# Kernel tuning notes

Hardware: AMD Instinct MI355X
Metric: run time of the kernel (lower is better)

The kernel has to match this reference:

```python
import jax, jax.numpy as jnp
import numpy as np

N, D, H = 8192, 1536, 1536


def setup_inputs() -> dict:
    key = jax.random.key(0)
    ks = jax.random.split(key, 7)
    def lin(kk, fan_in, fan_out):
        lim = 1.0 / np.sqrt(fan_in)
        return jax.random.uniform(kk, (fan_in, fan_out), jnp.float32, -lim, lim)
    return {
        "mentions": jax.random.normal(ks[0], (N, D), jnp.float32),
        "W0": lin(ks[1], D, H),
        "b0": jnp.zeros((H,), jnp.float32),
        "W1": lin(ks[2], H, H),
        "b1": jnp.zeros((H,), jnp.float32),
        "Wout": lin(ks[3], H, 1),
        "bout": jnp.zeros((1,), jnp.float32),
        "k": 50,
    }


def reference(mentions, W0, b0, W1, b1, Wout, bout, k):
    # MLP (dropout is identity at eval time); LeakyReLU slope 0.01 (torch default)
    h = jax.nn.leaky_relu(mentions @ W0 + b0, negative_slope=0.01)
    h = jax.nn.leaky_relu(h @ W1 + b1, negative_slope=0.01)
    s = (h @ Wout + bout).squeeze(-1)  # [N] per-mention scores
    n = s.shape[0]
    idx = jnp.arange(n)
    # pair_mask[i,j] = log(i - j > 0): 0 where j < i (valid antecedent), -inf otherwise
    pair_mask = jnp.where(idx[:, None] > idx[None, :], 0.0, -jnp.inf).astype(s.dtype)
    # scores_ij[i,j] = s[j] + s[i] + mask
    scores_ij = s[None, :] + s[:, None] + pair_mask
    top_scores, indices = jax.lax.top_k(scores_ij, min(int(k), n))
    return top_scores, indices
```

## Files before the change

### kernel.cpp

```cpp
#include <hip/hip_runtime.h>
#include <math.h>
#include <float.h>

#define BM 128
#define BN 128
#define BK 16
#define TM 8
#define TN 8
#define LDA_S (BM + 4)
#define LDB_S (BN + 16)

__device__ __forceinline__ int bpad(int c) { return c + ((c >> 5) << 2); }

__global__ __launch_bounds__(256) void sgemm_bias_act(
    const float* __restrict__ A, const float* __restrict__ W,
    const float* __restrict__ bias, float* __restrict__ C,
    int M, int K, int N)
{
    __shared__ float As[BK * LDA_S];
    __shared__ float Bs[BK * LDB_S];

    const int tid = threadIdx.x;
    const int bm = blockIdx.x;
    const int bn = blockIdx.y;

    const int tn = tid & 15;
    const int tm = tid >> 4;
    const int row0 = tm * TM;
    const int col0 = tn * TN;
    const int cs0 = bpad(col0);

    const int lr  = tid >> 2;
    const int lc4 = (tid & 3) << 2;
    const int br  = tid >> 5;
    const int bc4 = (tid & 31) << 2;
    const int bcs = bpad(bc4);

    const float* Ag = A + (size_t)(bm * BM) * K;
    const float* Wg = W + (size_t)bn * BN;

    float acc[TM][TN];
#pragma unroll
    for (int i = 0; i < TM; ++i)
#pragma unroll
        for (int j = 0; j < TN; ++j) acc[i][j] = 0.f;

    float4 a0 = *(const float4*)(Ag + (size_t)lr * K + lc4);
    float4 a1 = *(const float4*)(Ag + (size_t)(lr + 64) * K + lc4);
    float4 b0 = *(const float4*)(Wg + (size_t)br * N + bc4);
    float4 b1 = *(const float4*)(Wg + (size_t)(br + 8) * N + bc4);

    for (int k0 = 0; k0 < K; k0 += BK) {
        __syncthreads();
        As[(lc4 + 0) * LDA_S + lr] = a0.x;
        As[(lc4 + 1) * LDA_S + lr] = a0.y;
        As[(lc4 + 2) * LDA_S + lr] = a0.z;
        As[(lc4 + 3) * LDA_S + lr] = a0.w;
        As[(lc4 + 0) * LDA_S + lr + 64] = a1.x;
        As[(lc4 + 1) * LDA_S + lr + 64] = a1.y;
        As[(lc4 + 2) * LDA_S + lr + 64] = a1.z;
        As[(lc4 + 3) * LDA_S + lr + 64] = a1.w;
        *(float4*)&Bs[br * LDB_S + bcs] = b0;
        *(float4*)&Bs[(br + 8) * LDB_S + bcs] = b1;
        __syncthreads();

        if (k0 + BK < K) {
            const int kn = k0 + BK;
            a0 = *(const float4*)(Ag + (size_t)lr * K + kn + lc4);
            a1 = *(const float4*)(Ag + (size_t)(lr + 64) * K + kn + lc4);
            b0 = *(const float4*)(Wg + (size_t)(kn + br) * N + bc4);
            b1 = *(const float4*)(Wg + (size_t)(kn + br + 8) * N + bc4);
        }

#pragma unroll
        for (int kk = 0; kk < BK; ++kk) {
            float4 av0 = *(const float4*)&As[kk * LDA_S + row0];
            float4 av1 = *(const float4*)&As[kk * LDA_S + row0 + 4];
            float4 bv0 = *(const float4*)&Bs[kk * LDB_S + cs0];
            float4 bv1 = *(const float4*)&Bs[kk * LDB_S + cs0 + 4];
            float a[TM] = {av0.x, av0.y, av0.z, av0.w, av1.x, av1.y, av1.z, av1.w};
            float b[TN] = {bv0.x, bv0.y, bv0.z, bv0.w, bv1.x, bv1.y, bv1.z, bv1.w};
#pragma unroll
            for (int i = 0; i < TM; ++i)
#pragma unroll
                for (int j = 0; j < TN; ++j)
                    acc[i][j] = fmaf(a[i], b[j], acc[i][j]);
        }
    }

    float bv[TN];
#pragma unroll
    for (int j = 0; j < TN; ++j) bv[j] = bias[bn * BN + col0 + j];
#pragma unroll
    for (int i = 0; i < TM; ++i) {
        float o[TN];
#pragma unroll
        for (int j = 0; j < TN; ++j) {
            float x = acc[i][j] + bv[j];
            o[j] = x > 0.f ? x : 0.01f * x;
        }
        float* Cp = C + (size_t)(bm * BM + row0 + i) * N + (size_t)bn * BN + col0;
        *(float4*)Cp       = make_float4(o[0], o[1], o[2], o[3]);
        *(float4*)(Cp + 4) = make_float4(o[4], o[5], o[6], o[7]);
    }
}

__global__ __launch_bounds__(256) void gemv_wout(
    const float* __restrict__ H, const float* __restrict__ Wout,
    const float* __restrict__ bout, float* __restrict__ s, int K)
{
    const int row  = blockIdx.x * 4 + (threadIdx.x >> 6);
    const int lane = threadIdx.x & 63;
    const float4* h = (const float4*)(H + (size_t)row * K);
    const float4* w = (const float4*)Wout;
    float acc = 0.f;
    const int nv = K >> 2;
#pragma unroll
    for (int t = lane; t < nv; t += 64) {
        float4 hv = h[t];
        float4 wv = w[t];
        acc += hv.x * wv.x + hv.y * wv.y + hv.z * wv.z + hv.w * wv.w;
    }
#pragma unroll
    for (int off = 32; off; off >>= 1) acc += __shfl_xor(acc, off);
    if (lane == 0) s[row] = acc + bout[0];
}

#define EMPTY_SENTINEL (-1.0e38f)
#define HEAP_SENTINEL  (-1e30f)

__global__ void chunk_sort(const float* __restrict__ s,
                           float* __restrict__ cval, int* __restrict__ cidx)
{
    const int lane = threadIdx.x;
    const int base = blockIdx.x * 64;
    float v  = s[base + lane];
    int   id = base + lane;
#pragma unroll
    for (int ksz = 2; ksz <= 64; ksz <<= 1) {
#pragma unroll
        for (int j = 32; j >= 1; j >>= 1) {
            if (j >= ksz) continue;
            float ov = __shfl_xor(v, j);
            int   oi = __shfl_xor(id, j);
            const bool lower    = ((lane & j) == 0);
            const bool dirDesc  = ((lane & ksz) == 0);
            const bool wantBig  = (lower == dirDesc);
            const bool mineBig  = (v > ov) || (v == ov && id < oi);
            const bool keepMine = (mineBig == wantBig);
            v  = keepMine ? v  : ov;
            id = keepMine ? id : oi;
        }
    }
    cval[base + lane] = v;
    cidx[base + lane] = id;
}

__global__ void prefix_merge(const float* __restrict__ cval,
                             const int* __restrict__ cidx,
                             float* __restrict__ qval, int* __restrict__ qidx,
                             int nchunks)
{
    const int lane = threadIdx.x;
    float v  = HEAP_SENTINEL;
    int   id = 0x3FFFFFFF;
    for (int c = 0; c < nchunks; ++c) {
        qval[c * 64 + lane] = v;
        qidx[c * 64 + lane] = id;
        float bv = cval[c * 64 + (63 - lane)];
        int   bi = cidx[c * 64 + (63 - lane)];
        const bool mineBig0 = (v > bv) || (v == bv && id < bi);
        v  = mineBig0 ? v  : bv;
        id = mineBig0 ? id : bi;
#pragma unroll
        for (int j = 32; j >= 1; j >>= 1) {
            float ov = __shfl_xor(v, j);
            int   oi = __shfl_xor(id, j);
            const bool lower    = ((lane & j) == 0);
            const bool mineBig  = (v > ov) || (v == ov && id < oi);
            const bool keepMine = (mineBig == lower);
            v  = keepMine ? v  : ov;
            id = keepMine ? id : oi;
        }
    }
}

__global__ void topk_replay(const float* __restrict__ s,
                            const float* __restrict__ qval,
                            const int* __restrict__ qidx,
                            float* __restrict__ out_scores,
                            float* __restrict__ out_idx, int k)
{
    const int lane = threadIdx.x;
    const int c = blockIdx.x;
    float val = qval[c * 64 + lane];
    int   idx = qidx[c * 64 + lane];
    const float sv = s[c * 64 + lane];

    for (int t = 0; t < 64; ++t) {
        const int i = c * 64 + t;
        const float si = __shfl(sv, t);
        if (lane < k) {
            const bool empty = (lane >= i);
            out_scores[(size_t)i * k + lane] = empty ? EMPTY_SENTINEL : (si + val);
            out_idx[(size_t)i * k + lane]    = (float)(empty ? lane : idx);
        }
        unsigned long long ge = __ballot(val >= si);
        int p = __popcll(ge);
        float upv = __shfl_up(val, 1);
        int   upi = __shfl_up(idx, 1);
        if (lane > p)       { val = upv; idx = upi; }
        else if (lane == p) { val = si;  idx = i;   }
    }
}

extern "C" void kernel_launch(void* const* d_in, const int* in_sizes, int n_in,
                              void* d_out, int out_size, void* d_ws, size_t ws_size,
                              hipStream_t stream)
{
    const float* mentions = (const float*)d_in[0];
    const float* W0   = (const float*)d_in[1];
    const float* b0   = (const float*)d_in[2];
    const float* W1   = (const float*)d_in[3];
    const float* b1   = (const float*)d_in[4];
    const float* Wout = (const float*)d_in[5];
    const float* bout = (const float*)d_in[6];

    const int D = 1536, H = 1536;
    const int M = in_sizes[0] / D;
    const int k = out_size / (2 * M);
    const int NCH = M / 64;

    float* h0   = (float*)d_ws;
    float* h1   = h0 + (size_t)M * H;
    float* sc   = h1 + (size_t)M * H;
    float* cval = sc + M;
    int*   cidx = (int*)(cval + M);
    float* qval = (float*)(cidx + M);
    int*   qidx = (int*)(qval + M);

    dim3 g1(M / BM, H / BN);
    sgemm_bias_act<<<g1, 256, 0, stream>>>(mentions, W0, b0, h0, M, D, H);
    sgemm_bias_act<<<g1, 256, 0, stream>>>(h0, W1, b1, h1, M, H, H);
    gemv_wout<<<M / 4, 256, 0, stream>>>(h1, Wout, bout, sc, H);

    chunk_sort<<<NCH, 64, 0, stream>>>(sc, cval, cidx);
    prefix_merge<<<1, 64, 0, stream>>>(cval, cidx, qval, qidx, NCH);

    float* out_scores = (float*)d_out;
    float* out_idx    = (float*)d_out + (size_t)M * k;
    topk_replay<<<NCH, 64, 0, stream>>>(sc, qval, qidx, out_scores, out_idx, k);
}
```

Baseline: 1.077 ms.

## Double-buffer shared memory tiles in SGEMM to cut per-iteration barriers

Shared-memory A/B tiles in the fp32 GEMM become double buffered. Each step stores the already-loaded next tile into the other buffer and issues global loads two tiles ahead, so only one barrier per k-step is needed instead of two. This reduces synchronisation overhead and overlaps global latency with the FMA loop, at the cost of twice the LDS use, which may reduce occupancy, and more live registers.

```diff
diff --git a/kernel.cpp b/kernel.cpp
--- a/kernel.cpp
+++ b/kernel.cpp
@@ -17,8 +17,8 @@
     const float* __restrict__ bias, float* __restrict__ C,
     int M, int K, int N)
 {
-    __shared__ float As[BK * LDA_S];
-    __shared__ float Bs[BK * LDB_S];
+    __shared__ float As[2][BK * LDA_S];
+    __shared__ float Bs[2][BK * LDB_S];
 
     const int tid = threadIdx.x;
     const int bm = blockIdx.x;
@@ -45,47 +45,63 @@
 #pragma unroll
         for (int j = 0; j < TN; ++j) acc[i][j] = 0.f;
 
-    float4 a0 = *(const float4*)(Ag + (size_t)lr * K + lc4);
-    float4 a1 = *(const float4*)(Ag + (size_t)(lr + 64) * K + lc4);
-    float4 b0 = *(const float4*)(Wg + (size_t)br * N + bc4);
-    float4 b1 = *(const float4*)(Wg + (size_t)(br + 8) * N + bc4);
-
+    float4 a0, a1, b0, b1;
+#define LOAD_TILE(k0_)                                                        \
+    do {                                                                      \
+        a0 = *(const float4*)(Ag + (size_t)lr * K + (k0_) + lc4);             \
+        a1 = *(const float4*)(Ag + (size_t)(lr + 64) * K + (k0_) + lc4);      \
+        b0 = *(const float4*)(Wg + (size_t)((k0_) + br) * N + bc4);           \
+        b1 = *(const float4*)(Wg + (size_t)((k0_) + br + 8) * N + bc4);       \
+    } while (0)
+
+#define STORE_TILE(buf_)                                                      \
+    do {                                                                      \
+        As[buf_][(lc4 + 0) * LDA_S + lr] = a0.x;                              \
+        As[buf_][(lc4 + 1) * LDA_S + lr] = a0.y;                              \
+        As[buf_][(lc4 + 2) * LDA_S + lr] = a0.z;                              \
+        As[buf_][(lc4 + 3) * LDA_S + lr] = a0.w;                              \
+        As[buf_][(lc4 + 0) * LDA_S + lr + 64] = a1.x;                         \
+        As[buf_][(lc4 + 1) * LDA_S + lr + 64] = a1.y;                         \
+        As[buf_][(lc4 + 2) * LDA_S + lr + 64] = a1.z;                         \
+        As[buf_][(lc4 + 3) * LDA_S + lr + 64] = a1.w;                         \
+        *(float4*)&Bs[buf_][br * LDB_S + bcs] = b0;                           \
+        *(float4*)&Bs[buf_][(br + 8) * LDB_S + bcs] = b1;                     \
+    } while (0)
+
+    LOAD_TILE(0);
+    STORE_TILE(0);
+    if (BK < K) LOAD_TILE(BK);
+    __syncthreads();
+
+    int cur = 0;
     for (int k0 = 0; k0 < K; k0 += BK) {
+        if (k0 + BK < K) STORE_TILE(cur ^ 1);
+        if (k0 + 2 * BK < K) LOAD_TILE(k0 + 2 * BK);
+        const float* Ac = As[cur];
+        const float* Bc = Bs[cur];
+#pragma unroll
+        for (int kk = 0; kk < BK; ++kk) {
+            const float4 av0 = *(const float4*)&Ac[kk * LDA_S + row0];
+            const float4 av1 = *(const float4*)&Ac[kk * LDA_S + row0 + 4];
+            const float4 bv0 = *(const float4*)&Bc[kk * LDB_S + cs0];
+            const float4 bv1 = *(const float4*)&Bc[kk * LDB_S + cs0 + 4];
+#define FMA_ROW(i, ax)                                                        \
+            acc[i][0] = fmaf(ax, bv0.x, acc[i][0]);                           \
+            acc[i][1] = fmaf(ax, bv0.y, acc[i][1]);                           \
+            acc[i][2] = fmaf(ax, bv0.z, acc[i][2]);                           \
+            acc[i][3] = fmaf(ax, bv0.w, acc[i][3]);                           \
+            acc[i][4] = fmaf(ax, bv1.x, acc[i][4]);                           \
+            acc[i][5] = fmaf(ax, bv1.y, acc[i][5]);                           \
+            acc[i][6] = fmaf(ax, bv1.z, acc[i][6]);                           \
+            acc[i][7] = fmaf(ax, bv1.w, acc[i][7])
+            FMA_ROW(0, av0.x); FMA_ROW(1, av0.y);
+            FMA_ROW(2, av0.z); FMA_ROW(3, av0.w);
+            FMA_ROW(4, av1.x); FMA_ROW(5, av1.y);
+            FMA_ROW(6, av1.z); FMA_ROW(7, av1.w);
+#undef FMA_ROW
+        }
         __syncthreads();
-        As[(lc4 + 0) * LDA_S + lr] = a0.x;
-        As[(lc4 + 1) * LDA_S + lr] = a0.y;
-        As[(lc4 + 2) * LDA_S + lr] = a0.z;
-        As[(lc4 + 3) * LDA_S + lr] = a0.w;
-        As[(lc4 + 0) * LDA_S + lr + 64] = a1.x;
-        As[(lc4 + 1) * LDA_S + lr + 64] = a1.y;
-        As[(lc4 + 2) * LDA_S + lr + 64] = a1.z;
-        As[(lc4 + 3) * LDA_S + lr + 64] = a1.w;
-        *(float4*)&Bs[br * LDB_S + bcs] = b0;
-        *(float4*)&Bs[(br + 8) * LDB_S + bcs] = b1;
-        __syncthreads();
-
-        if (k0 + BK < K) {
-            const int kn = k0 + BK;
-            a0 = *(const float4*)(Ag + (size_t)lr * K + kn + lc4);
-            a1 = *(const float4*)(Ag + (size_t)(lr + 64) * K + kn + lc4);
-            b0 = *(const float4*)(Wg + (size_t)(kn + br) * N + bc4);
-            b1 = *(const float4*)(Wg + (size_t)(kn + br + 8) * N + bc4);
-        }
-
-#pragma unroll
-        for (int kk = 0; kk < BK; ++kk) {
-            float4 av0 = *(const float4*)&As[kk * LDA_S + row0];
-            float4 av1 = *(const float4*)&As[kk * LDA_S + row0 + 4];
-            float4 bv0 = *(const float4*)&Bs[kk * LDB_S + cs0];
-            float4 bv1 = *(const float4*)&Bs[kk * LDB_S + cs0 + 4];
-            float a[TM] = {av0.x, av0.y, av0.z, av0.w, av1.x, av1.y, av1.z, av1.w};
-            float b[TN] = {bv0.x, bv0.y, bv0.z, bv0.w, bv1.x, bv1.y, bv1.z, bv1.w};
-#pragma unroll
-            for (int i = 0; i < TM; ++i)
-#pragma unroll
-                for (int j = 0; j < TN; ++j)
-                    acc[i][j] = fmaf(a[i], b[j], acc[i][j]);
-        }
+        cur ^= 1;
     }
 
     float bv[TN];
@@ -103,6 +119,8 @@
         *(float4*)Cp       = make_float4(o[0], o[1], o[2], o[3]);
         *(float4*)(Cp + 4) = make_float4(o[4], o[5], o[6], o[7]);
     }
+#undef LOAD_TILE
+#undef STORE_TILE
 }
 
 __global__ __launch_bounds__(256) void gemv_wout(
```

Result: no change. 1.083 ms (+0.6%).
